# Kernel optimization log

Hardware: AMD Instinct MI355X
Metric: run time of the kernel (lower is better)

## Reference

```python
import jax, jax.numpy as jnp
import numpy as np

# Concrete MACE layer instantiation: hidden irreps = F x (0e + 1o)
N, E, F, R, S, H = 20000, 320000, 64, 8, 10, 64
P = 5                      # CG tensor-product paths for (0e+1o) x (0e+1o)
AVG_NEIGH = 16.0
INV_SQRT3 = 1.0 / np.sqrt(3.0).astype(np.float32)
INV_SQRT2 = 1.0 / np.sqrt(2.0).astype(np.float32)


def setup_inputs() -> dict:
    key = jax.random.key(0)
    ks = jax.random.split(key, 24)
    rn = lambda k, shp, sc=1.0: jax.random.normal(k, shp, dtype=jnp.float32) * sc
    y = jax.random.normal(ks[2], (E, 3), dtype=jnp.float32)
    Y1 = y / jnp.linalg.norm(y, axis=-1, keepdims=True)  # unit spherical harmonics l=1
    return dict(
        s=rn(ks[0], (N, F)),                 # scalar node feats (0e)
        v=rn(ks[1], (N, F, 3)),              # vector node feats (1o)
        Y1=Y1,
        edge_feats=rn(ks[3], (E, R)),        # radial basis
        node_specie=jax.random.randint(ks[4], (N,), 0, S),
        senders=jax.random.randint(ks[5], (E,), 0, N),
        receivers=jax.random.randint(ks[6], (E,), 0, N),
        W_lin_s=rn(ks[7], (F, F), F ** -0.5),
        W_lin_v=rn(ks[8], (F, F), F ** -0.5),
        W_sc_s=rn(ks[9], (S, F, F), F ** -0.5),   # species-dependent skip
        W_sc_v=rn(ks[10], (S, F, F), F ** -0.5),
        W_rad1=rn(ks[11], (R, H), R ** -0.5),     # radial MLP
        W_rad2=rn(ks[12], (H, P * F), H ** -0.5),
        W_int_s=rn(ks[13], (F, F), F ** -0.5),    # post-aggregation linear
        W_int_v=rn(ks[14], (F, F), F ** -0.5),
        w_prod_s=rn(ks[15], (S, 5, F)),           # product-basis species weights (0e out)
        w_prod_v=rn(ks[16], (S, 4, F)),           # product-basis species weights (1o out)
        W_prod_s=rn(ks[17], (F, F), F ** -0.5),
        W_prod_v=rn(ks[18], (F, F), F ** -0.5),
        W_read=rn(ks[19], (F, 1), F ** -0.5),     # linear readout to 0e
    )


def reference(s, v, Y1, edge_feats, node_specie, senders, receivers,
              W_lin_s, W_lin_v, W_sc_s, W_sc_v, W_rad1, W_rad2,
              W_int_s, W_int_v, w_prod_s, w_prod_v, W_prod_s, W_prod_v, W_read):
    n = s.shape[0]
    # --- interaction block: linear up ---
    s1 = s @ W_lin_s                              # [N,F]
    v1 = jnp.einsum('nfc,fg->ngc', v, W_lin_v)    # [N,F,3]
    # species-dependent residual skip connection
    sc_s = jnp.einsum('nf,nfg->ng', s, W_sc_s[node_specie])
    sc_v = jnp.einsum('nfc,nfg->ngc', v, W_sc_v[node_specie])
    # radial MLP -> per-edge, per-path, per-channel tensor-product weights
    h = jax.nn.silu(edge_feats @ W_rad1)
    tw = (h @ W_rad2).reshape(-1, P, F)           # [E,P,F]
    # gather sender features onto edges
    ss = s1[senders]                              # [E,F]
    vs = v1[senders]                              # [E,F,3]
    # CG tensor product with edge spherical harmonics (Y0 == const)
    dot = jnp.einsum('efc,ec->ef', vs, Y1)        # 1o x 1o -> 0e
    crs = jnp.cross(vs, Y1[:, None, :])           # 1o x 1o -> 1o
    m_s = tw[:, 0] * ss + tw[:, 1] * dot * INV_SQRT3                     # [E,F]
    m_v = (tw[:, 2, :, None] * ss[..., None] * Y1[:, None, :]            # 0e x 1o -> 1o
           + tw[:, 3, :, None] * vs                                      # 1o x 0e -> 1o
           + tw[:, 4, :, None] * crs * INV_SQRT2)                        # [E,F,3]
    # scatter-sum over edges to receiver nodes
    A_s = jax.ops.segment_sum(m_s, receivers, num_segments=n)
    A_v = jax.ops.segment_sum(m_v, receivers, num_segments=n)
    # linear to interaction irreps + neighbor normalization (epsilon is None)
    inv = 1.0 / jnp.sqrt(jnp.asarray(AVG_NEIGH, s.dtype))
    A_s = (A_s @ W_int_s) * inv
    A_v = jnp.einsum('nfc,fg->ngc', A_v, W_int_v) * inv
    # --- equivariant product basis (symmetric contraction, correlation=3) ---
    ws = w_prod_s[node_specie]                    # [N,5,F]
    wv = w_prod_v[node_specie]                    # [N,4,F]
    d = jnp.sum(A_v * A_v, axis=-1)               # v.v invariant [N,F]
    B_s = (ws[:, 0] * A_s + ws[:, 1] * A_s * A_s + ws[:, 2] * d
           + ws[:, 3] * A_s ** 3 + ws[:, 4] * A_s * d)
    B_v = (wv[:, 0] + wv[:, 1] * A_s + wv[:, 2] * A_s * A_s + wv[:, 3] * d)[..., None] * A_v
    s_out = B_s @ W_prod_s + sc_s
    v_out = jnp.einsum('nfc,fg->ngc', B_v, W_prod_v) + sc_v
    # --- linear readout (not last layer): invariant per-node output ---
    node_outputs = s_out @ W_read                 # [N,1]
    return node_outputs, s_out, v_out
```

## Files before the change

### kernel.cpp

```cpp
#include <hip/hip_runtime.h>

#define NNODES 20000
#define NEDGES 320000
#define NTILES 1260

typedef __attribute__((ext_vector_type(8))) short short8;
typedef __attribute__((ext_vector_type(4))) float float4v;
typedef _Float16 half2v __attribute__((ext_vector_type(2)));

#define CW2   0
#define CWls  2560
#define CWlv  3072
#define CWis  3584
#define CWiv  4096
#define CWps  4608
#define CWpv  5120
#define CWss  5632
#define CWsv  10752
#define NCHUNK_TOT 15872

__device__ __forceinline__ float bitsf(unsigned u){ union{unsigned u; float f;} x; x.u=u; return x.f; }
__device__ __forceinline__ float b2f(unsigned short u){ return bitsf(((unsigned)u)<<16); }
__device__ __forceinline__ unsigned short f2b(float f){
    union{float f; unsigned u;} x; x.f=f;
    unsigned r = x.u + 0x7fffu + ((x.u>>16)&1u);
    return (unsigned short)(r>>16);
}
__device__ __forceinline__ short8 pack8(const float* f){
    short8 r;
    #pragma unroll
    for (int j=0;j<8;++j) r[j] = (short)f2b(f[j]);
    return r;
}

__constant__ float kINV_SQRT3 = 0.5773502691896258f;
__constant__ float kINV_SQRT2 = 0.7071067811865476f;
__constant__ float kINV_AVG   = 0.25f;

__global__ __launch_bounds__(256) void kprep(
    const int* __restrict__ specie,
    const float* __restrict__ Wr2,
    const float* __restrict__ Wls, const float* __restrict__ Wlv,
    const float* __restrict__ Wis, const float* __restrict__ Wiv,
    const float* __restrict__ Wps, const float* __restrict__ Wpv,
    const float* __restrict__ Wss, const float* __restrict__ Wsv,
    unsigned short* __restrict__ P,
    int* __restrict__ perm, int* __restrict__ tspec,
    int* __restrict__ ecnt)
{
    const int tid = threadIdx.x;
    for (int i = blockIdx.x*256 + tid; i < NNODES; i += 63*256) ecnt[i] = 0;

    if (blockIdx.x == 0){
        __shared__ int cnt[10], base[10], ntl[10], cur[10];
        if (tid < 10) cnt[tid] = 0;
        __syncthreads();
        for (int n = tid; n < NNODES; n += 256) atomicAdd(&cnt[specie[n]], 1);
        __syncthreads();
        if (tid == 0){
            int b = 0;
            for (int sp = 0; sp < 10; ++sp){
                base[sp] = b; cur[sp] = b;
                ntl[sp] = (cnt[sp] + 15) >> 4;
                b += ntl[sp] << 4;
            }
        }
        __syncthreads();
        for (int i = tid; i < NTILES*16; i += 256) perm[i] = -1;
        for (int t = tid; t < NTILES; t += 256){
            int sp = 0;
            #pragma unroll
            for (int k = 0; k < 10; ++k)
                if (t >= (base[k] >> 4) && t < (base[k] >> 4) + ntl[k]) sp = k;
            tspec[t] = sp;
        }
        __syncthreads();
        for (int n = tid; n < NNODES; n += 256){
            int slot = atomicAdd(&cur[specie[n]], 1);
            perm[slot] = n;
        }
        return;
    }
    const int c = (blockIdx.x - 1)*256 + tid;
    if (c >= NCHUNK_TOT) return;
    unsigned short t[8];
    if (c < 2560){
        const int nt = c >> 7, ks = (c >> 6) & 1, ln = c & 63;
        const int col = nt*16 + (ln & 15);
        const int jb  = ks*32 + ((ln >> 4) & 3)*8;
        #pragma unroll
        for (int jj = 0; jj < 8; ++jj) t[jj] = f2b(Wr2[(jb+jj)*320 + col]);
    } else {
        int c2 = c - 2560;
        const float* src;
        if      (c2 <  512){ src = Wls; }
        else if (c2 < 1024){ src = Wlv; c2 -= 512; }
        else if (c2 < 1536){ src = Wis; c2 -= 1024; }
        else if (c2 < 2048){ src = Wiv; c2 -= 1536; }
        else if (c2 < 2560){ src = Wps; c2 -= 2048; }
        else if (c2 < 3072){ src = Wpv; c2 -= 2560; }
        else if (c2 < 8192){ src = Wss; c2 -= 3072; }
        else               { src = Wsv; c2 -= 8192; }
        const int grp = c2 >> 9, loc = c2 & 511;
        const int nt = loc >> 7, ks = (loc >> 6) & 1, ln = loc & 63;
        const int col  = nt*16 + (ln & 15);
        const int row0 = grp*64 + ks*32 + ((ln>>4)&3)*8;
        #pragma unroll
        for (int jj = 0; jj < 8; ++jj) t[jj] = f2b(src[(row0+jj)*64 + col]);
    }
    unsigned* d = (unsigned*)(P + (size_t)c*8);
    d[0] = (unsigned)t[0] | ((unsigned)t[1]<<16);
    d[1] = (unsigned)t[2] | ((unsigned)t[3]<<16);
    d[2] = (unsigned)t[4] | ((unsigned)t[5]<<16);
    d[3] = (unsigned)t[6] | ((unsigned)t[7]<<16);
}

__global__ __launch_bounds__(256) void knodeA2(
    const float* __restrict__ s, const float* __restrict__ v,
    const unsigned short* __restrict__ P,
    const int* __restrict__ receivers, int* __restrict__ ecnt,
    unsigned short* __restrict__ s1, unsigned short* __restrict__ v1,
    float4v* __restrict__ AhZ)
{
    float4v zz = {0.f,0.f,0.f,0.f};
    for (int i = blockIdx.x*256 + threadIdx.x; i < NNODES*32; i += 313*256) AhZ[i] = zz;
    for (int e = blockIdx.x*256 + threadIdx.x; e < NEDGES; e += 313*256)
        atomicAdd(&ecnt[receivers[e]], 1);

    const int w = threadIdx.x >> 6, lane = threadIdx.x & 63;
    const int t = blockIdx.x*4 + w;
    if (t >= 1250) return;
    const int mcol = lane & 15, quad = lane >> 4;
    const int node = t*16 + mcol;
    const short8* PB = (const short8*)P;

    short8 fS[2], fV[3][2];
    #pragma unroll
    for (int ks = 0; ks < 2; ++ks){
        const int k0 = ks*32 + quad*8;
        float ts[8];
        { float4v a = *(const float4v*)&s[node*64 + k0];
          float4v b = *(const float4v*)&s[node*64 + k0 + 4];
          #pragma unroll
          for (int j = 0; j < 4; ++j){ ts[j] = a[j]; ts[4+j] = b[j]; } }
        fS[ks] = pack8(ts);
        float tv[24];
        #pragma unroll
        for (int q = 0; q < 6; ++q){
            float4v x = *(const float4v*)&v[(node*64 + k0)*3 + q*4];
            #pragma unroll
            for (int j = 0; j < 4; ++j) tv[q*4+j] = x[j];
        }
        #pragma unroll
        for (int c = 0; c < 3; ++c){
            float tc[8];
            #pragma unroll
            for (int j = 0; j < 8; ++j) tc[j] = tv[j*3 + c];
            fV[c][ks] = pack8(tc);
        }
    }
    float4v z = {0.f,0.f,0.f,0.f};
    #pragma unroll
    for (int nt = 0; nt < 4; ++nt){
        float4v aS = __builtin_amdgcn_mfma_f32_16x16x32_bf16(fS[0], PB[CWls+(nt*2+0)*64+lane], z, 0,0,0);
        aS = __builtin_amdgcn_mfma_f32_16x16x32_bf16(fS[1], PB[CWls+(nt*2+1)*64+lane], aS, 0,0,0);
        float4v aV[3];
        #pragma unroll
        for (int c = 0; c < 3; ++c){
            aV[c] = __builtin_amdgcn_mfma_f32_16x16x32_bf16(fV[c][0], PB[CWlv+(nt*2+0)*64+lane], z, 0,0,0);
            aV[c] = __builtin_amdgcn_mfma_f32_16x16x32_bf16(fV[c][1], PB[CWlv+(nt*2+1)*64+lane], aV[c], 0,0,0);
        }
        const int g = nt*16 + mcol;
        #pragma unroll
        for (int r = 0; r < 4; ++r){
            const int nr = t*16 + quad*4 + r;
            s1[nr*64 + g] = f2b(aS[r]);
            #pragma unroll
            for (int c = 0; c < 3; ++c) v1[(nr*3+c)*64 + g] = f2b(aV[c][r]);
        }
    }
}

__global__ __launch_bounds__(256) void kscan(int* __restrict__ ecnt)
{
    __shared__ int part[256];
    const int tid  = threadIdx.x;
    const int base = tid*79;
    int sum = 0;
    #pragma unroll 1
    for (int i = 0; i < 79; ++i){
        int idx = base + i;
        if (idx < NNODES) sum += ecnt[idx];
    }
    part[tid] = sum;
    __syncthreads();
    if (tid == 0){
        int acc = 0;
        #pragma unroll 1
        for (int i = 0; i < 256; ++i){ int c = part[i]; part[i] = acc; acc += c; }
    }
    __syncthreads();
    int run = part[tid];
    #pragma unroll 1
    for (int i = 0; i < 79; ++i){
        int idx = base + i;
        if (idx < NNODES){ int c = ecnt[idx]; ecnt[idx] = run; run += c; }
    }
}

__global__ __launch_bounds__(256) void kscat(
    const int* __restrict__ receivers, int* __restrict__ ecur, int* __restrict__ eperm)
{
    const int e = blockIdx.x*256 + threadIdx.x;
    if (e >= NEDGES) return;
    const int pos = atomicAdd(&ecur[receivers[e]], 1);
    eperm[pos] = e;
}

__global__ __launch_bounds__(256) void kedge2(
    const float* __restrict__ Y1, const float* __restrict__ ef,
    const int* __restrict__ senders, const int* __restrict__ receivers,
    const float* __restrict__ Wr1, const unsigned short* __restrict__ W2s,
    const unsigned short* __restrict__ s1, const unsigned short* __restrict__ v1,
    const int* __restrict__ eperm,
    half2v* __restrict__ Ah)
{
    __shared__ unsigned short hlds[64*72];
    __shared__ unsigned short twlds[64*330];
    const int lane = threadIdx.x & 63;
    const int w    = threadIdx.x >> 6;
    const int ew   = blockIdx.x*64 + w*16;

    int epreg = 0;
    if (lane < 16) epreg = eperm[ew + lane];
    const int  eme = __shfl(epreg, lane >> 2);
    const float efa = ef[eme*8 + (lane&3)*2];
    const float efb = ef[eme*8 + (lane&3)*2 + 1];

    float w1r[8];
    #pragma unroll
    for (int r = 0; r < 8; ++r) w1r[r] = Wr1[r*64 + lane];

    float y0r = 0.f, y1r = 0.f, y2r = 0.f;
    int   sndreg = 0, rcvreg = 0;
    if (lane < 16){
        y0r = Y1[epreg*3 + 0];
        y1r = Y1[epreg*3 + 1];
        y2r = Y1[epreg*3 + 2];
        sndreg = senders[epreg];
        rcvreg = receivers[epreg];
    }

    #pragma unroll
    for (int e16 = 0; e16 < 16; ++e16){
        float hj = 0.f;
        #pragma unroll
        for (int r = 0; r < 8; ++r)
            hj += __shfl((r&1) ? efb : efa, e16*4 + (r>>1)) * w1r[r];
        hj = hj / (1.f + __expf(-hj));
        hlds[(w*16 + e16)*72 + lane] = f2b(hj);
    }
    __syncthreads();

    short8 a0 = *(const short8*)&hlds[(w*16 + (lane&15))*72 +      (lane>>4)*8];
    short8 a1 = *(const short8*)&hlds[(w*16 + (lane&15))*72 + 32 + (lane>>4)*8];
    float4v acc[20];
    #pragma unroll
    for (int nt = 0; nt < 20; ++nt){
        short8 b0 = *(const short8*)&W2s[((nt*2+0)*64 + lane)*8];
        short8 b1 = *(const short8*)&W2s[((nt*2+1)*64 + lane)*8];
        float4v z = {0.f, 0.f, 0.f, 0.f};
        acc[nt] = __builtin_amdgcn_mfma_f32_16x16x32_bf16(a0, b0, z, 0, 0, 0);
        acc[nt] = __builtin_amdgcn_mfma_f32_16x16x32_bf16(a1, b1, acc[nt], 0, 0, 0);
    }
    #pragma unroll
    for (int nt = 0; nt < 20; ++nt){
        const int col = nt*16 + (lane & 15);
        #pragma unroll
        for (int r = 0; r < 4; ++r){
            const int erow = w*16 + (lane>>4)*4 + r;
            twlds[erow*330 + col] = f2b(acc[nt][r]);
        }
    }

    int   cur = -1;
    float aS = 0.f, aV0 = 0.f, aV1 = 0.f, aV2 = 0.f;
    for (int e16 = 0; e16 < 16; ++e16){
        const int erow = w*16 + e16;
        float tw0 = b2f(twlds[erow*330 +   0 + lane]);
        float tw1 = b2f(twlds[erow*330 +  64 + lane]);
        float tw2 = b2f(twlds[erow*330 + 128 + lane]);
        float tw3 = b2f(twlds[erow*330 + 192 + lane]);
        float tw4 = b2f(twlds[erow*330 + 256 + lane]);
        const int snd = __shfl(sndreg, e16);
        const int rcv = __shfl(rcvreg, e16);
        float y0 = __shfl(y0r, e16);
        float y1 = __shfl(y1r, e16);
        float y2 = __shfl(y2r, e16);
        float ss  = b2f(s1[snd*64 + lane]);
        float vs0 = b2f(v1[(snd*3+0)*64 + lane]);
        float vs1 = b2f(v1[(snd*3+1)*64 + lane]);
        float vs2 = b2f(v1[(snd*3+2)*64 + lane]);
        float dot = vs0*y0 + vs1*y1 + vs2*y2;
        float c0 = vs1*y2 - vs2*y1;
        float c1 = vs2*y0 - vs0*y2;
        float c2 = vs0*y1 - vs1*y0;
        float ms  = tw0*ss + tw1*dot*kINV_SQRT3;
        float t2s = tw2*ss, t4 = tw4*kINV_SQRT2;
        float mv0 = t2s*y0 + tw3*vs0 + t4*c0;
        float mv1 = t2s*y1 + tw3*vs1 + t4*c1;
        float mv2 = t2s*y2 + tw3*vs2 + t4*c2;
        if (rcv != cur){
            if (cur >= 0){
                half2v p01 = { (_Float16)aS,  (_Float16)aV0 };
                half2v p23 = { (_Float16)aV1, (_Float16)aV2 };
                __builtin_amdgcn_global_atomic_fadd_v2f16(&Ah[cur*128 + lane],      p01);
                __builtin_amdgcn_global_atomic_fadd_v2f16(&Ah[cur*128 + 64 + lane], p23);
            }
            cur = rcv;
            aS = 0.f; aV0 = 0.f; aV1 = 0.f; aV2 = 0.f;
        }
        aS += ms; aV0 += mv0; aV1 += mv1; aV2 += mv2;
    }
    if (cur >= 0){
        half2v p01 = { (_Float16)aS,  (_Float16)aV0 };
        half2v p23 = { (_Float16)aV1, (_Float16)aV2 };
        __builtin_amdgcn_global_atomic_fadd_v2f16(&Ah[cur*128 + lane],      p01);
        __builtin_amdgcn_global_atomic_fadd_v2f16(&Ah[cur*128 + 64 + lane], p23);
    }
}

__global__ __launch_bounds__(256) void knodeC2(
    const float* __restrict__ s, const float* __restrict__ v,
    const half2v* __restrict__ Ah,
    const unsigned short* __restrict__ P,
    const int* __restrict__ perm, const int* __restrict__ tspec,
    const float* __restrict__ wps, const float* __restrict__ wpv,
    const float* __restrict__ Wread,
    float* __restrict__ out)
{
    __shared__ unsigned short Bt[4][4][16*72];
    const int w = threadIdx.x >> 6, lane = threadIdx.x & 63;
    const int t = blockIdx.x*4 + w;
    if (t >= NTILES) return;
    const int mcol = lane & 15, quad = lane >> 4;
    const int spec = tspec[t];
    const int nA   = perm[t*16 + mcol];
    const short8* PB = (const short8*)P;
    const int sb = CWss + spec*512, vb = CWsv + spec*512;

    short8 fAs[2], fAv[3][2], fS[2], fV[3][2];
    if (nA >= 0){
        #pragma unroll
        for (int ks = 0; ks < 2; ++ks){
            const int k0 = ks*32 + quad*8;
            half2v pa[8], pb[8];
            *(float4v*)&pa[0] = *(const float4v*)&Ah[nA*128 + k0];
            *(float4v*)&pa[4] = *(const float4v*)&Ah[nA*128 + k0 + 4];
            *(float4v*)&pb[0] = *(const float4v*)&Ah[nA*128 + 64 + k0];
            *(float4v*)&pb[4] = *(const float4v*)&Ah[nA*128 + 64 + k0 + 4];
            float as_[8], a0_[8], a1_[8], a2_[8];
            #pragma unroll
            for (int j = 0; j < 8; ++j){
                as_[j] = (float)pa[j].x; a0_[j] = (float)pa[j].y;
                a1_[j] = (float)pb[j].x; a2_[j] = (float)pb[j].y;
            }
            fAs[ks] = pack8(as_); fAv[0][ks] = pack8(a0_);
            fAv[1][ks] = pack8(a1_); fAv[2][ks] = pack8(a2_);
            float ts[8];
            { float4v a = *(const float4v*)&s[nA*64 + k0];
              float4v b = *(const float4v*)&s[nA*64 + k0 + 4];
              #pragma unroll
              for (int j = 0; j < 4; ++j){ ts[j] = a[j]; ts[4+j] = b[j]; } }
            fS[ks] = pack8(ts);
            float tv[24];
            #pragma unroll
            for (int q = 0; q < 6; ++q){
                float4v x = *(const float4v*)&v[(nA*64 + k0)*3 + q*4];
                #pragma unroll
                for (int j = 0; j < 4; ++j) tv[q*4+j] = x[j];
            }
            #pragma unroll
            for (int c = 0; c < 3; ++c){
                float tc[8];
                #pragma unroll
                for (int j = 0; j < 8; ++j) tc[j] = tv[j*3 + c];
                fV[c][ks] = pack8(tc);
            }
        }
    } else {
        short8 z8 = {};
        #pragma unroll
        for (int ks = 0; ks < 2; ++ks){
            fAs[ks] = z8; fS[ks] = z8;
            #pragma unroll
            for (int c = 0; c < 3; ++c){ fAv[c][ks] = z8; fV[c][ks] = z8; }
        }
    }

    float4v z = {0.f,0.f,0.f,0.f};
    float4v scS[4], scV[3][4];
    #pragma unroll
    for (int nt = 0; nt < 4; ++nt){
        float4v Ais = __builtin_amdgcn_mfma_f32_16x16x32_bf16(fAs[0], PB[CWis+(nt*2+0)*64+lane], z, 0,0,0);
        Ais = __builtin_amdgcn_mfma_f32_16x16x32_bf16(fAs[1], PB[CWis+(nt*2+1)*64+lane], Ais, 0,0,0);
        float4v Aiv[3];
        #pragma unroll
        for (int c = 0; c < 3; ++c){
            Aiv[c] = __builtin_amdgcn_mfma_f32_16x16x32_bf16(fAv[c][0], PB[CWiv+(nt*2+0)*64+lane], z, 0,0,0);
            Aiv[c] = __builtin_amdgcn_mfma_f32_16x16x32_bf16(fAv[c][1], PB[CWiv+(nt*2+1)*64+lane], Aiv[c], 0,0,0);
        }
        scS[nt] = __builtin_amdgcn_mfma_f32_16x16x32_bf16(fS[0], PB[sb+(nt*2+0)*64+lane], z, 0,0,0);
        scS[nt] = __builtin_amdgcn_mfma_f32_16x16x32_bf16(fS[1], PB[sb+(nt*2+1)*64+lane], scS[nt], 0,0,0);
        #pragma unroll
        for (int c = 0; c < 3; ++c){
            scV[c][nt] = __builtin_amdgcn_mfma_f32_16x16x32_bf16(fV[c][0], PB[vb+(nt*2+0)*64+lane], z, 0,0,0);
            scV[c][nt] = __builtin_amdgcn_mfma_f32_16x16x32_bf16(fV[c][1], PB[vb+(nt*2+1)*64+lane], scV[c][nt], 0,0,0);
        }
        const int g = nt*16 + mcol;
        float w0 = wps[spec*320 +   0 + g], w1 = wps[spec*320 +  64 + g];
        float w2 = wps[spec*320 + 128 + g], w3 = wps[spec*320 + 192 + g];
        float w4 = wps[spec*320 + 256 + g];
        float u0 = wpv[spec*256 +   0 + g], u1 = wpv[spec*256 +  64 + g];
        float u2 = wpv[spec*256 + 128 + g], u3 = wpv[spec*256 + 192 + g];
        #pragma unroll
        for (int r = 0; r < 4; ++r){
            float A  = Ais[r]    * kINV_AVG;
            float a0 = Aiv[0][r] * kINV_AVG;
            float a1 = Aiv[1][r] * kINV_AVG;
            float a2 = Aiv[2][r] * kINV_AVG;
            float d   = a0*a0 + a1*a1 + a2*a2;
            float as2 = A*A;
            float Bs  = w0*A + w1*as2 + w2*d + w3*as2*A + w4*A*d;
            float gg  = u0 + u1*A + u2*as2 + u3*d;
            const int row = quad*4 + r;
            Bt[w][0][row*72 + g] = f2b(Bs);
            Bt[w][1][row*72 + g] = f2b(gg*a0);
            Bt[w][2][row*72 + g] = f2b(gg*a1);
            Bt[w][3][row*72 + g] = f2b(gg*a2);
        }
    }

    short8 bS[2], bV[3][2];
    #pragma unroll
    for (int ks = 0; ks < 2; ++ks){
        bS[ks] = *(const short8*)&Bt[w][0][mcol*72 + ks*32 + quad*8];
        #pragma unroll
        for (int c = 0; c < 3; ++c)
            bV[c][ks] = *(const short8*)&Bt[w][1+c][mcol*72 + ks*32 + quad*8];
    }

    float* out_node = out;
    float* out_s    = out + NNODES;
    float* out_v    = out + NNODES + NNODES*64;
    int ndr[4];
    #pragma unroll
    for (int r = 0; r < 4; ++r) ndr[r] = perm[t*16 + quad*4 + r];
    float4v rd = {0.f,0.f,0.f,0.f};
    #pragma unroll
    for (int nt = 0; nt < 4; ++nt){
        float4v oS = scS[nt];
        oS = __builtin_amdgcn_mfma_f32_16x16x32_bf16(bS[0], PB[CWps+(nt*2+0)*64+lane], oS, 0,0,0);
        oS = __builtin_amdgcn_mfma_f32_16x16x32_bf16(bS[1], PB[CWps+(nt*2+1)*64+lane], oS, 0,0,0);
        float4v oV[3];
        #pragma unroll
        for (int c = 0; c < 3; ++c){
            oV[c] = scV[c][nt];
            oV[c] = __builtin_amdgcn_mfma_f32_16x16x32_bf16(bV[c][0], PB[CWpv+(nt*2+0)*64+lane], oV[c], 0,0,0);
            oV[c] = __builtin_amdgcn_mfma_f32_16x16x32_bf16(bV[c][1], PB[CWpv+(nt*2+1)*64+lane], oV[c], 0,0,0);
        }
        const int g = nt*16 + mcol;
        float wr = Wread[g];
        #pragma unroll
        for (int r = 0; r < 4; ++r){
            if (ndr[r] >= 0){
                out_s[ndr[r]*64 + g] = oS[r];
                #pragma unroll
                for (int c = 0; c < 3; ++c) out_v[(ndr[r]*64 + g)*3 + c] = oV[c][r];
            }
            rd[r] += oS[r] * wr;
        }
    }
    #pragma unroll
    for (int off = 1; off < 16; off <<= 1){
        #pragma unroll
        for (int r = 0; r < 4; ++r) rd[r] += __shfl_xor(rd[r], off);
    }
    if (mcol == 0){
        #pragma unroll
        for (int r = 0; r < 4; ++r) if (ndr[r] >= 0) out_node[ndr[r]] = rd[r];
    }
}

extern "C" void kernel_launch(void* const* d_in, const int* in_sizes, int n_in,
                              void* d_out, int out_size, void* d_ws, size_t ws_size,
                              hipStream_t stream)
{
    (void)in_sizes; (void)n_in; (void)out_size; (void)ws_size;
    const float* s    = (const float*)d_in[0];
    const float* v    = (const float*)d_in[1];
    const float* Y1   = (const float*)d_in[2];
    const float* ef   = (const float*)d_in[3];
    const int* specie = (const int*)d_in[4];
    const int* senders   = (const int*)d_in[5];
    const int* receivers = (const int*)d_in[6];
    const float* Wls  = (const float*)d_in[7];
    const float* Wlv  = (const float*)d_in[8];
    const float* Wss  = (const float*)d_in[9];
    const float* Wsv  = (const float*)d_in[10];
    const float* Wr1  = (const float*)d_in[11];
    const float* Wr2  = (const float*)d_in[12];
    const float* Wis  = (const float*)d_in[13];
    const float* Wiv  = (const float*)d_in[14];
    const float* wps  = (const float*)d_in[15];
    const float* wpv  = (const float*)d_in[16];
    const float* Wps  = (const float*)d_in[17];
    const float* Wpv  = (const float*)d_in[18];
    const float* Wrd  = (const float*)d_in[19];

    float* out = (float*)d_out;
    unsigned short* t_s1 = (unsigned short*)(out + NNODES);
    unsigned short* t_v1 = t_s1 + NNODES*64;
    int* ecnt  = (int*)(out + 2600000);
    int* eperm = (int*)(out + 2624000);

    char* ws = (char*)d_ws;
    unsigned short* P = (unsigned short*)ws;
    half2v* Ah  = (half2v*)(ws + 262144);
    int* perm   = (int*)(ws + 10502144);
    int* tspec  = (int*)(ws + 10582784);

    kprep<<<63, 256, 0, stream>>>(specie, Wr2, Wls, Wlv, Wis, Wiv, Wps, Wpv, Wss, Wsv,
                                  P, perm, tspec, ecnt);
    knodeA2<<<313, 256, 0, stream>>>(s, v, P, receivers, ecnt, t_s1, t_v1, (float4v*)Ah);
    kscan<<<1, 256, 0, stream>>>(ecnt);
    kscat<<<1250, 256, 0, stream>>>(receivers, ecnt, eperm);
    kedge2<<<5000, 256, 0, stream>>>(Y1, ef, senders, receivers, Wr1, P + CW2*8, t_s1, t_v1, eperm, Ah);
    knodeC2<<<315, 256, 0, stream>>>(s, v, Ah, P, perm, tspec, wps, wpv, Wrd, out);
}
```

Measured before the change: 374.0 us.

## Interleave sender features, prefetch gathers, fp32 atomics, vectorize scan

Packs s1 and the three v1 components into one interleaved bf16x4 array so each sender gather is a single 8-byte load. All 16 gathers per wave are issued up front, ahead of the radial MLP. The fp16x2 aggregation buffer becomes fp32 with four scalar atomics per flush, which doubles the accumulator memory and atomic count in exchange for accuracy. The scan kernel is vectorized with int4 loads, and kedge2 gets an occupancy hint of 3 blocks.

```diff
diff --git a/kernel.cpp b/kernel.cpp
--- a/kernel.cpp
+++ b/kernel.cpp
@@ -6,7 +6,8 @@
 
 typedef __attribute__((ext_vector_type(8))) short short8;
 typedef __attribute__((ext_vector_type(4))) float float4v;
-typedef _Float16 half2v __attribute__((ext_vector_type(2)));
+typedef __attribute__((ext_vector_type(4))) unsigned short ushort4v;
+typedef __attribute__((ext_vector_type(4))) int int4v;
 
 #define CW2   0
 #define CWls  2560
@@ -31,6 +32,9 @@
     #pragma unroll
     for (int j=0;j<8;++j) r[j] = (short)f2b(f[j]);
     return r;
+}
+__device__ __forceinline__ void atomAddF32(float* p, float v){
+    asm volatile("global_atomic_add_f32 %0, %1, off" :: "v"(p), "v"(v) : "memory");
 }
 
 __constant__ float kINV_SQRT3 = 0.5773502691896258f;
@@ -119,11 +123,11 @@
     const float* __restrict__ s, const float* __restrict__ v,
     const unsigned short* __restrict__ P,
     const int* __restrict__ receivers, int* __restrict__ ecnt,
-    unsigned short* __restrict__ s1, unsigned short* __restrict__ v1,
+    unsigned short* __restrict__ sv1,
     float4v* __restrict__ AhZ)
 {
     float4v zz = {0.f,0.f,0.f,0.f};
-    for (int i = blockIdx.x*256 + threadIdx.x; i < NNODES*32; i += 313*256) AhZ[i] = zz;
+    for (int i = blockIdx.x*256 + threadIdx.x; i < NNODES*64; i += 313*256) AhZ[i] = zz;
     for (int e = blockIdx.x*256 + threadIdx.x; e < NEDGES; e += 313*256)
         atomicAdd(&ecnt[receivers[e]], 1);
 
@@ -174,9 +178,8 @@
         #pragma unroll
         for (int r = 0; r < 4; ++r){
             const int nr = t*16 + quad*4 + r;
-            s1[nr*64 + g] = f2b(aS[r]);
-            #pragma unroll
-            for (int c = 0; c < 3; ++c) v1[(nr*3+c)*64 + g] = f2b(aV[c][r]);
+            ushort4v pk = { f2b(aS[r]), f2b(aV[0][r]), f2b(aV[1][r]), f2b(aV[2][r]) };
+            *(ushort4v*)&sv1[(size_t)(nr*64 + g)*4] = pk;
         }
     }
 }
@@ -184,27 +187,35 @@
 __global__ __launch_bounds__(256) void kscan(int* __restrict__ ecnt)
 {
     __shared__ int part[256];
-    const int tid  = threadIdx.x;
-    const int base = tid*79;
+    const int tid = threadIdx.x;
+    int4v* e4 = (int4v*)ecnt;
+    const int b4 = tid*20;
+    int4v c[20];
+    #pragma unroll
+    for (int i = 0; i < 20; ++i){
+        int4v zi = {0,0,0,0};
+        c[i] = (b4 + i < 5000) ? e4[b4 + i] : zi;
+    }
     int sum = 0;
-    #pragma unroll 1
-    for (int i = 0; i < 79; ++i){
-        int idx = base + i;
-        if (idx < NNODES) sum += ecnt[idx];
-    }
+    #pragma unroll
+    for (int i = 0; i < 20; ++i) sum += c[i][0] + c[i][1] + c[i][2] + c[i][3];
     part[tid] = sum;
     __syncthreads();
     if (tid == 0){
         int acc = 0;
         #pragma unroll 1
-        for (int i = 0; i < 256; ++i){ int c = part[i]; part[i] = acc; acc += c; }
+        for (int i = 0; i < 256; ++i){ int t = part[i]; part[i] = acc; acc += t; }
     }
     __syncthreads();
     int run = part[tid];
-    #pragma unroll 1
-    for (int i = 0; i < 79; ++i){
-        int idx = base + i;
-        if (idx < NNODES){ int c = ecnt[idx]; ecnt[idx] = run; run += c; }
+    #pragma unroll
+    for (int i = 0; i < 20; ++i){
+        int4v o;
+        o[0] = run; run += c[i][0];
+        o[1] = run; run += c[i][1];
+        o[2] = run; run += c[i][2];
+        o[3] = run; run += c[i][3];
+        if (b4 + i < 5000) e4[b4 + i] = o;
     }
 }
 
@@ -217,13 +228,13 @@
     eperm[pos] = e;
 }
 
-__global__ __launch_bounds__(256) void kedge2(
+__global__ __launch_bounds__(256, 3) void kedge2(
     const float* __restrict__ Y1, const float* __restrict__ ef,
     const int* __restrict__ senders, const int* __restrict__ receivers,
     const float* __restrict__ Wr1, const unsigned short* __restrict__ W2s,
-    const unsigned short* __restrict__ s1, const unsigned short* __restrict__ v1,
+    const unsigned short* __restrict__ sv1,
     const int* __restrict__ eperm,
-    half2v* __restrict__ Ah)
+    float* __restrict__ Ahf)
 {
     __shared__ unsigned short hlds[64*72];
     __shared__ unsigned short twlds[64*330];
@@ -236,10 +247,6 @@
     const int  eme = __shfl(epreg, lane >> 2);
     const float efa = ef[eme*8 + (lane&3)*2];
     const float efb = ef[eme*8 + (lane&3)*2 + 1];
-
-    float w1r[8];
-    #pragma unroll
-    for (int r = 0; r < 8; ++r) w1r[r] = Wr1[r*64 + lane];
 
     float y0r = 0.f, y1r = 0.f, y2r = 0.f;
     int   sndreg = 0, rcvreg = 0;
@@ -251,6 +258,17 @@
         rcvreg = receivers[epreg];
     }
 
+    ushort4v svp[16];
+    #pragma unroll
+    for (int e16 = 0; e16 < 16; ++e16){
+        const int snd = __shfl(sndreg, e16);
+        svp[e16] = *(const ushort4v*)&sv1[(size_t)(snd*64 + lane)*4];
+    }
+
+    float w1r[8];
+    #pragma unroll
+    for (int r = 0; r < 8; ++r) w1r[r] = Wr1[r*64 + lane];
+
     #pragma unroll
     for (int e16 = 0; e16 < 16; ++e16){
         float hj = 0.f;
@@ -285,6 +303,7 @@
 
     int   cur = -1;
     float aS = 0.f, aV0 = 0.f, aV1 = 0.f, aV2 = 0.f;
+    #pragma unroll
     for (int e16 = 0; e16 < 16; ++e16){
         const int erow = w*16 + e16;
         float tw0 = b2f(twlds[erow*330 +   0 + lane]);
@@ -292,15 +311,15 @@
         float tw2 = b2f(twlds[erow*330 + 128 + lane]);
         float tw3 = b2f(twlds[erow*330 + 192 + lane]);
         float tw4 = b2f(twlds[erow*330 + 256 + lane]);
-        const int snd = __shfl(sndreg, e16);
         const int rcv = __shfl(rcvreg, e16);
         float y0 = __shfl(y0r, e16);
         float y1 = __shfl(y1r, e16);
         float y2 = __shfl(y2r, e16);
-        float ss  = b2f(s1[snd*64 + lane]);
-        float vs0 = b2f(v1[(snd*3+0)*64 + lane]);
-        float vs1 = b2f(v1[(snd*3+1)*64 + lane]);
-        float vs2 = b2f(v1[(snd*3+2)*64 + lane]);
+        const ushort4v q = svp[e16];
+        float ss  = b2f(q[0]);
+        float vs0 = b2f(q[1]);
+        float vs1 = b2f(q[2]);
+        float vs2 = b2f(q[3]);
         float dot = vs0*y0 + vs1*y1 + vs2*y2;
         float c0 = vs1*y2 - vs2*y1;
         float c1 = vs2*y0 - vs0*y2;
@@ -312,10 +331,11 @@
         float mv2 = t2s*y2 + tw3*vs2 + t4*c2;
         if (rcv != cur){
             if (cur >= 0){
-                half2v p01 = { (_Float16)aS,  (_Float16)aV0 };
-                half2v p23 = { (_Float16)aV1, (_Float16)aV2 };
-                __builtin_amdgcn_global_atomic_fadd_v2f16(&Ah[cur*128 + lane],      p01);
-                __builtin_amdgcn_global_atomic_fadd_v2f16(&Ah[cur*128 + 64 + lane], p23);
+                float* base = &Ahf[(size_t)cur*256 + lane];
+                atomAddF32(base,       aS);
+                atomAddF32(base + 64,  aV0);
+                atomAddF32(base + 128, aV1);
+                atomAddF32(base + 192, aV2);
             }
             cur = rcv;
             aS = 0.f; aV0 = 0.f; aV1 = 0.f; aV2 = 0.f;
@@ -323,16 +343,17 @@
         aS += ms; aV0 += mv0; aV1 += mv1; aV2 += mv2;
     }
     if (cur >= 0){
-        half2v p01 = { (_Float16)aS,  (_Float16)aV0 };
-        half2v p23 = { (_Float16)aV1, (_Float16)aV2 };
-        __builtin_amdgcn_global_atomic_fadd_v2f16(&Ah[cur*128 + lane],      p01);
-        __builtin_amdgcn_global_atomic_fadd_v2f16(&Ah[cur*128 + 64 + lane], p23);
+        float* base = &Ahf[(size_t)cur*256 + lane];
+        atomAddF32(base,       aS);
+        atomAddF32(base + 64,  aV0);
+        atomAddF32(base + 128, aV1);
+        atomAddF32(base + 192, aV2);
     }
 }
 
 __global__ __launch_bounds__(256) void knodeC2(
     const float* __restrict__ s, const float* __restrict__ v,
-    const half2v* __restrict__ Ah,
+    const float* __restrict__ Ahf,
     const unsigned short* __restrict__ P,
     const int* __restrict__ perm, const int* __restrict__ tspec,
     const float* __restrict__ wps, const float* __restrict__ wpv,
@@ -354,17 +375,24 @@
         #pragma unroll
         for (int ks = 0; ks < 2; ++ks){
             const int k0 = ks*32 + quad*8;
-            half2v pa[8], pb[8];
-            *(float4v*)&pa[0] = *(const float4v*)&Ah[nA*128 + k0];
-            *(float4v*)&pa[4] = *(const float4v*)&Ah[nA*128 + k0 + 4];
-            *(float4v*)&pb[0] = *(const float4v*)&Ah[nA*128 + 64 + k0];
-            *(float4v*)&pb[4] = *(const float4v*)&Ah[nA*128 + 64 + k0 + 4];
+            const float* ab = &Ahf[(size_t)nA*256 + k0];
             float as_[8], a0_[8], a1_[8], a2_[8];
-            #pragma unroll
-            for (int j = 0; j < 8; ++j){
-                as_[j] = (float)pa[j].x; a0_[j] = (float)pa[j].y;
-                a1_[j] = (float)pb[j].x; a2_[j] = (float)pb[j].y;
-            }
+            { float4v x0 = *(const float4v*)&ab[0];
+              float4v x1 = *(const float4v*)&ab[4];
+              #pragma unroll
+              for (int j = 0; j < 4; ++j){ as_[j] = x0[j]; as_[4+j] = x1[j]; } }
+            { float4v x0 = *(const float4v*)&ab[64];
+              float4v x1 = *(const float4v*)&ab[68];
+              #pragma unroll
+              for (int j = 0; j < 4; ++j){ a0_[j] = x0[j]; a0_[4+j] = x1[j]; } }
+            { float4v x0 = *(const float4v*)&ab[128];
+              float4v x1 = *(const float4v*)&ab[132];
+              #pragma unroll
+              for (int j = 0; j < 4; ++j){ a1_[j] = x0[j]; a1_[4+j] = x1[j]; } }
+            { float4v x0 = *(const float4v*)&ab[192];
+              float4v x1 = *(const float4v*)&ab[196];
+              #pragma unroll
+              for (int j = 0; j < 4; ++j){ a2_[j] = x0[j]; a2_[4+j] = x1[j]; } }
             fAs[ks] = pack8(as_); fAv[0][ks] = pack8(a0_);
             fAv[1][ks] = pack8(a1_); fAv[2][ks] = pack8(a2_);
             float ts[8];
@@ -519,22 +547,21 @@
     const float* Wrd  = (const float*)d_in[19];
 
     float* out = (float*)d_out;
-    unsigned short* t_s1 = (unsigned short*)(out + NNODES);
-    unsigned short* t_v1 = t_s1 + NNODES*64;
+    unsigned short* t_sv = (unsigned short*)(out + NNODES);
     int* ecnt  = (int*)(out + 2600000);
     int* eperm = (int*)(out + 2624000);
 
     char* ws = (char*)d_ws;
     unsigned short* P = (unsigned short*)ws;
-    half2v* Ah  = (half2v*)(ws + 262144);
-    int* perm   = (int*)(ws + 10502144);
-    int* tspec  = (int*)(ws + 10582784);
+    float* Ahf  = (float*)(ws + 262144);
+    int* perm   = (int*)(ws + 20742144);
+    int* tspec  = (int*)(ws + 20822784);
 
     kprep<<<63, 256, 0, stream>>>(specie, Wr2, Wls, Wlv, Wis, Wiv, Wps, Wpv, Wss, Wsv,
                                   P, perm, tspec, ecnt);
-    knodeA2<<<313, 256, 0, stream>>>(s, v, P, receivers, ecnt, t_s1, t_v1, (float4v*)Ah);
+    knodeA2<<<313, 256, 0, stream>>>(s, v, P, receivers, ecnt, t_sv, (float4v*)Ahf);
     kscan<<<1, 256, 0, stream>>>(ecnt);
     kscat<<<1250, 256, 0, stream>>>(receivers, ecnt, eperm);
-    kedge2<<<5000, 256, 0, stream>>>(Y1, ef, senders, receivers, Wr1, P + CW2*8, t_s1, t_v1, eperm, Ah);
-    knodeC2<<<315, 256, 0, stream>>>(s, v, Ah, P, perm, tspec, wps, wpv, Wrd, out);
-}
+    kedge2<<<5000, 256, 0, stream>>>(Y1, ef, senders, receivers, Wr1, P + CW2*8, t_sv, eperm, Ahf);
+    knodeC2<<<315, 256, 0, stream>>>(s, v, Ahf, P, perm, tspec, wps, wpv, Wrd, out);
+}
```

New measurement: 324.0 us. 1.15x faster.
